# Optimization experiments

Hardware: AMD Instinct MI355X
Metric: run time of the kernel (lower is better)

The kernel has to match this reference:

```python
import math
import jax, jax.numpy as jnp
import numpy as np

NUM_HEADS = 16
D_MODEL = 1024
WINDOW = 512


def alibi_slopes(num_heads):
    # 1 / ((2**8)**((i+1)/num_heads))  for i in range(num_heads)
    x = (2.0 ** 8) ** (1.0 / num_heads)
    return jnp.asarray([1.0 / x ** (i + 1) for i in range(num_heads)], dtype=jnp.float32)


def setup_inputs() -> dict:
    key = jax.random.key(0)
    k1, k2 = jax.random.split(key)
    x = jax.random.normal(k1, (1, 4096, D_MODEL), dtype=jnp.float32)
    # scale weight like a trained init so softmax isn't saturated
    w_kqv = jax.random.normal(k2, (D_MODEL, 3 * D_MODEL), dtype=jnp.float32) * 0.02
    return {"x": x, "w_kqv": w_kqv}


def reference(x, w_kqv):
    B, S, D = x.shape
    H = NUM_HEADS
    hd = D // H
    scale = math.sqrt(D)  # module scales by sqrt(d_model), not sqrt(head_dim)

    kqv = x @ w_kqv                       # [B, S, 3D]
    k, q, v = jnp.split(kqv, 3, axis=-1)  # chunk order: key, query, value
    k = k.reshape(B, S, H, hd).transpose(0, 2, 1, 3)  # [B, H, S, hd]
    q = q.reshape(B, S, H, hd).transpose(0, 2, 1, 3)
    v = v.reshape(B, S, H, hd).transpose(0, 2, 1, 3)

    # ALiBi bias: m_h * (j - i)
    pos = jnp.arange(S)
    rel = pos[None, :] - pos[:, None]                  # [S, S] = x - y
    bias = alibi_slopes(H)[:, None, None] * rel.astype(jnp.float32)  # [H, S, S]

    score = jnp.einsum("bhqd,bhkd->bhqk", q, k) / scale + bias[None]

    # causal sliding-window mask: allow 0 <= i - j <= WINDOW
    dist = pos[:, None] - pos[None, :]                 # i - j
    mask = (dist >= 0) & (dist <= WINDOW)              # [S, S]
    score = jnp.where(mask[None, None], score, -jnp.inf)

    attn = jax.nn.softmax(score, axis=-1)
    out = jnp.einsum("bhqk,bhkd->bhqd", attn, v)       # [B, H, S, hd]
    out = out.transpose(0, 2, 1, 3).reshape(B, S, D)
    return out
```

## Files before the change

kernel.cpp:

```cpp
#include <hip/hip_runtime.h>
#include <hip/hip_bf16.h>

#define SEQ   4096
#define DM    1024
#define NH    16
#define HD    64
#define N3    3072
#define WIN   512

#define LOG2E 1.4426950408889634f

typedef __attribute__((ext_vector_type(8))) short short8;
typedef __attribute__((ext_vector_type(4))) short short4v;
typedef __attribute__((ext_vector_type(4))) float float4v;

__device__ __forceinline__ float bf16_bits_to_float(unsigned short u) {
  return __uint_as_float(((unsigned int)u) << 16);
}

typedef __attribute__((address_space(3))) void lds_void_t;
typedef __attribute__((address_space(1))) const void gbl_void_t;
__device__ __forceinline__ void async_copy16(void* lds_dst, const void* g_src) {
  __builtin_amdgcn_global_load_lds((gbl_void_t*)g_src, (lds_void_t*)lds_dst,
                                   16, 0, 0);
}

template <int NT>
__device__ __forceinline__ int detect_fp32(const unsigned short* __restrict__ probe,
                                           float* red) {
  const int t = threadIdx.x;
  float mx = 0.0f;
#pragma unroll
  for (int p = 0; p < 8; ++p) {
    float v = bf16_bits_to_float(probe[(t * 8 + p) * 2]);
    if (v != v) v = 1e38f;
    mx = fmaxf(mx, fabsf(v));
  }
  red[t] = mx;
  __syncthreads();
  for (int s = NT / 2; s > 0; s >>= 1) {
    if (t < s) red[t] = fmaxf(red[t], red[t + s]);
    __syncthreads();
  }
  const int fl = red[0] > 100.0f ? 1 : 0;
  __syncthreads();
  return fl;
}

__device__ __forceinline__ int detect_fp32_wave(
    const unsigned short* __restrict__ probe) {
  const int lane = threadIdx.x & 63;
  float mx = 0.0f;
#pragma unroll
  for (int p = 0; p < 8; ++p) {
    float v = bf16_bits_to_float(probe[(lane * 8 + p) * 2]);
    if (v != v) v = 1e38f;
    mx = fmaxf(mx, fabsf(v));
  }
  return __any(mx > 100.0f) ? 1 : 0;
}

__global__ __launch_bounds__(256) void prep(
    const void* __restrict__ x, const void* __restrict__ w,
    __hip_bfloat16* __restrict__ xb, __hip_bfloat16* __restrict__ wt) {
  __shared__ __hip_bfloat16 tile[64][66];
  __shared__ float red[256];
  const int t = threadIdx.x;
  if (blockIdx.x < 2048) {
    const int fl = detect_fp32<256>((const unsigned short*)x, red);
    const int i0 = (blockIdx.x * 256 + t) * 8;
    if (fl) {
      const float* xf = (const float*)x + i0;
      float4 f0 = *(const float4*)(xf);
      float4 f1 = *(const float4*)(xf + 4);
      __hip_bfloat16 tmp[8];
      tmp[0] = __float2bfloat16(f0.x); tmp[1] = __float2bfloat16(f0.y);
      tmp[2] = __float2bfloat16(f0.z); tmp[3] = __float2bfloat16(f0.w);
      tmp[4] = __float2bfloat16(f1.x); tmp[5] = __float2bfloat16(f1.y);
      tmp[6] = __float2bfloat16(f1.z); tmp[7] = __float2bfloat16(f1.w);
      *(uint4*)&xb[i0] = *(const uint4*)tmp;
    } else {
      *(uint4*)&xb[i0] = *(const uint4*)((const __hip_bfloat16*)x + i0);
    }
  } else {
    const int bid = blockIdx.x - 2048;
    const int fl = detect_fp32<256>((const unsigned short*)w, red);
    const int n0 = (bid % 48) * 64;
    const int k0 = (bid / 48) * 64;
    const int tx = t & 63, ty0 = t >> 6;
    if (fl) {
      const float* wf = (const float*)w;
#pragma unroll
      for (int p = 0; p < 16; ++p) {
        int row = ty0 + p * 4;
        tile[row][tx] = __float2bfloat16(wf[(k0 + row) * N3 + n0 + tx]);
      }
    } else {
      const __hip_bfloat16* wb = (const __hip_bfloat16*)w;
#pragma unroll
      for (int p = 0; p < 16; ++p) {
        int row = ty0 + p * 4;
        tile[row][tx] = wb[(k0 + row) * N3 + n0 + tx];
      }
    }
    __syncthreads();
#pragma unroll
    for (int r = 0; r < 2; ++r) {
      int oe = r * 2048 + t * 8;
      int nr = oe >> 6, kc = oe & 63;
      __hip_bfloat16 v[8];
#pragma unroll
      for (int e = 0; e < 8; ++e) v[e] = tile[kc + e][nr];
      *(uint4*)&wt[(n0 + nr) * DM + k0 + kc] = *(const uint4*)v;
    }
  }
}

__global__ __launch_bounds__(512, 2) void gemm_kqv(
    const __hip_bfloat16* __restrict__ A,
    const __hip_bfloat16* __restrict__ BT,
    __hip_bfloat16* __restrict__ C) {
  __shared__ __align__(16) __hip_bfloat16 As[2][2][128 * 32];
  __shared__ __align__(16) __hip_bfloat16 Bs[2][192 * 64];

  const int flat = blockIdx.y * 16 + blockIdx.x;
  const int swz  = (flat & 7) * 64 + (flat >> 3);
  const int m0 = (swz >> 4) * 128;
  const int n0 = (swz & 15) * 192;

  const int t = threadIdx.x;
  const int wave = t >> 6, lane = t & 63;
  const int wm = wave >> 2, wn = wave & 3;
  const int l15 = lane & 15, quad = lane >> 4;

  const int arow = t >> 2;
  const int acol = ((t & 3) ^ (arow & 3)) * 8;
  const long aoff = (long)(m0 + arow) * DM + acol;
  const int brow = t >> 3;
  const int bcol = ((t & 7) ^ (brow & 7)) * 8;
  const long boff0 = (long)(n0 +       brow) * DM + bcol;
  const long boff1 = (long)(n0 +  64 + brow) * DM + bcol;
  const long boff2 = (long)(n0 + 128 + brow) * DM + bcol;
  const int ldst = t * 16;

#define STAGE_B(buf, kt) do { \
    const int ko_ = (kt) * 64; \
    async_copy16((char*)Bs[buf]         + ldst, &BT[boff0 + ko_]); \
    async_copy16((char*)Bs[buf] +  8192 + ldst, &BT[boff1 + ko_]); \
    async_copy16((char*)Bs[buf] + 16384 + ldst, &BT[boff2 + ko_]); } while (0)
#define STAGE_A(buf, kt) do { \
    const int ko_ = (kt) * 64; \
    async_copy16((char*)As[buf][0] + ldst, &A[aoff + ko_]); \
    async_copy16((char*)As[buf][1] + ldst, &A[aoff + ko_ + 32]); } while (0)

  float4v acc[4][3] = {};

  STAGE_B(0, 0); STAGE_A(0, 0);
  asm volatile("s_waitcnt vmcnt(0)" ::: "memory");
  __builtin_amdgcn_s_barrier();

  for (int kt = 0; kt < 16; ++kt) {
    const int P = kt & 1, N = P ^ 1;
    short8 a[4], b[3];

#pragma unroll
    for (int h = 0; h < 2; ++h) {
      const char* Ap = (const char*)As[P][h];
      const char* Bp = (const char*)Bs[P];
#pragma unroll
      for (int mi = 0; mi < 4; ++mi) {
        const int row = wm * 64 + mi * 16 + l15;
        a[mi] = *(const short8*)(Ap + row * 64 + ((quad ^ (row & 3)) << 4));
      }
#pragma unroll
      for (int ni = 0; ni < 3; ++ni) {
        const int row = wn * 48 + ni * 16 + l15;
        b[ni] = *(const short8*)(Bp + row * 128 +
                                 ((((h << 2) + quad) ^ (row & 7)) << 4));
      }
      if (h == 0) {
        if (kt < 15) {
          STAGE_B(N, kt + 1);
          asm volatile("s_waitcnt vmcnt(3)" ::: "memory");
        } else {
          asm volatile("s_waitcnt vmcnt(0)" ::: "memory");
        }
      } else {
        if (kt < 15) STAGE_A(N, kt + 1);
        asm volatile("s_waitcnt vmcnt(1)" ::: "memory");
      }
      __builtin_amdgcn_s_barrier();
      __builtin_amdgcn_s_setprio(1);
#pragma unroll
      for (int mi = 0; mi < 4; ++mi)
#pragma unroll
        for (int ni = 0; ni < 3; ++ni)
          acc[mi][ni] = __builtin_amdgcn_mfma_f32_16x16x32_bf16(
              a[mi], b[ni], acc[mi][ni], 0, 0, 0);
      __builtin_amdgcn_s_setprio(0);
      __builtin_amdgcn_s_barrier();
    }
  }
#undef STAGE_A
#undef STAGE_B

#pragma unroll
  for (int mi = 0; mi < 4; ++mi)
#pragma unroll
    for (int ni = 0; ni < 3; ++ni)
#pragma unroll
      for (int r = 0; r < 4; ++r) {
        int row = m0 + wm * 64 + mi * 16 + quad * 4 + r;
        int col = n0 + wn * 48 + ni * 16 + l15;
        C[row * N3 + col] = __float2bfloat16(acc[mi][ni][r]);
      }
}

#define SWZ(row) (((((row) ^ ((row) >> 3))) & 7) << 4)

__global__ __launch_bounds__(256, 4) void attn(
    const __hip_bfloat16* __restrict__ kqv,
    const unsigned short* __restrict__ xprobe,
    void* __restrict__ out) {
  __shared__ __align__(16) __hip_bfloat16 Ks[2][64 * 64];
  __shared__ __align__(16) __hip_bfloat16 Vt[2][64 * 64];
  __shared__ __align__(16) __hip_bfloat16 Ps[64 * 64];

  const int fl = detect_fp32_wave(xprobe);
  const int h  = blockIdx.y;
  const int bx = blockIdx.x;
  const int i0 = 64 * ((bx & 7) * 8 + (bx >> 3));
  const int t    = threadIdx.x;
  const int wave = t >> 6, lane = t & 63;
  const int l15 = lane & 15, quad = lane >> 4;
  const float nslope2 = -exp2f(-0.5f * (float)(h + 1)) * LOG2E;
  const float qscale  = LOG2E / 32.0f;

  short8 aq[2];
#pragma unroll
  for (int ks2 = 0; ks2 < 2; ++ks2)
    aq[ks2] = *(const short8*)&kqv[(i0 + wave * 16 + l15) * N3 + DM + h * HD +
                                   ks2 * 32 + quad * 8];

  float4v o[4] = {};
  float lsum[4] = {0.f, 0.f, 0.f, 0.f};

  const int jlo  = max(0, i0 - WIN);
  const int nblk = (i0 + 64 - jlo) >> 6;

  const int krow0 = t >> 3, krow1 = (t >> 3) + 32, kd0 = (t & 7) * 8;
  const int kdst0 = krow0 * 128 + ((kd0 * 2) ^ SWZ(krow0));
  const int kdst1 = krow1 * 128 + ((kd0 * 2) ^ SWZ(krow1));
  const int rbase = t >> 3;
  const int vd0   = (t & 7) * 8;
  const int kA    = (rbase & 15) + ((rbase >> 4) << 5);
  const int vsig2 = ((rbase & 15) * 8) + ((rbase >> 4) * 4);

  uint4 kregA, kregB, vregA, vregB;
  kregA = *(const uint4*)&kqv[(jlo + krow0) * N3 + h * HD + kd0];
  kregB = *(const uint4*)&kqv[(jlo + krow1) * N3 + h * HD + kd0];
  vregA = *(const uint4*)&kqv[(jlo + kA) * N3 + 2 * DM + h * HD + vd0];
  vregB = *(const uint4*)&kqv[(jlo + kA + 16) * N3 + 2 * DM + h * HD + vd0];

  {
    *(uint4*)((char*)Ks[0] + kdst0) = kregA;
    *(uint4*)((char*)Ks[0] + kdst1) = kregB;
    const unsigned short* pa = (const unsigned short*)&vregA;
    const unsigned short* pb = (const unsigned short*)&vregB;
#pragma unroll
    for (int e = 0; e < 8; ++e) {
      unsigned int pack = (unsigned int)pa[e] | ((unsigned int)pb[e] << 16);
      *(unsigned int*)((char*)Vt[0] + (vd0 + e) * 128 + (vsig2 ^ SWZ(vd0 + e))) = pack;
    }
  }
  if (nblk > 1) {
    const int jn = jlo + 64;
    kregA = *(const uint4*)&kqv[(jn + krow0) * N3 + h * HD + kd0];
    kregB = *(const uint4*)&kqv[(jn + krow1) * N3 + h * HD + kd0];
    vregA = *(const uint4*)&kqv[(jn + kA) * N3 + 2 * DM + h * HD + vd0];
    vregB = *(const uint4*)&kqv[(jn + kA + 16) * N3 + 2 * DM + h * HD + vd0];
  }
  __syncthreads();

  for (int b = 0; b < nblk; ++b) {
    const int cur = b & 1, nxt = cur ^ 1;

    float4v sacc[4] = {};
#pragma unroll
    for (int ks2 = 0; ks2 < 2; ++ks2)
#pragma unroll
      for (int nt = 0; nt < 4; ++nt) {
        const int row = nt * 16 + l15;
        short8 bk = *(const short8*)((const char*)Ks[cur] + row * 128 +
                                     ((ks2 * 64 + quad * 16) ^ SWZ(row)));
        sacc[nt] = __builtin_amdgcn_mfma_f32_16x16x32_bf16(aq[ks2], bk, sacc[nt], 0, 0, 0);
      }

    const int dbase = (i0 + wave * 16 + quad * 4) - (jlo + b * 64 + l15);
    const float s16 = nslope2 * -16.0f;
#pragma unroll
    for (int r = 0; r < 4; ++r) {
      float bias = nslope2 * (float)(dbase + r);
      int rel = dbase + r;
      short4v pk;
      float ls = 0.0f;
#pragma unroll
      for (int nt = 0; nt < 4; ++nt) {
        float x = fmaf(sacc[nt][r], qscale, bias);
        x = ((unsigned)rel <= (unsigned)WIN) ? x : -200.0f;
        __hip_bfloat16 hb = __float2bfloat16(exp2f(x));
        unsigned short bits = *reinterpret_cast<const unsigned short*>(&hb);
        pk[nt] = (short)bits;
        ls += bf16_bits_to_float(bits);
        bias += s16;
        rel -= 16;
      }
      lsum[r] += ls;
      const int prow = wave * 16 + quad * 4 + r;
      *(short4v*)((char*)Ps + prow * 128 + ((l15 * 8) ^ SWZ(prow))) = pk;
    }

    if (b + 1 < nblk) {
      *(uint4*)((char*)Ks[nxt] + kdst0) = kregA;
      *(uint4*)((char*)Ks[nxt] + kdst1) = kregB;
      const unsigned short* pa = (const unsigned short*)&vregA;
      const unsigned short* pb = (const unsigned short*)&vregB;
#pragma unroll
      for (int e = 0; e < 8; ++e) {
        unsigned int pack = (unsigned int)pa[e] | ((unsigned int)pb[e] << 16);
        *(unsigned int*)((char*)Vt[nxt] + (vd0 + e) * 128 + (vsig2 ^ SWZ(vd0 + e))) = pack;
      }
      if (b + 2 < nblk) {
        const int jn = jlo + (b + 2) * 64;
        kregA = *(const uint4*)&kqv[(jn + krow0) * N3 + h * HD + kd0];
        kregB = *(const uint4*)&kqv[(jn + krow1) * N3 + h * HD + kd0];
        vregA = *(const uint4*)&kqv[(jn + kA) * N3 + 2 * DM + h * HD + vd0];
        vregB = *(const uint4*)&kqv[(jn + kA + 16) * N3 + 2 * DM + h * HD + vd0];
      }
    }

#pragma unroll
    for (int ks = 0; ks < 64; ks += 32) {
      const int prow = wave * 16 + l15;
      short8 ap = *(const short8*)((const char*)Ps + prow * 128 +
                                   ((ks * 2 + quad * 16) ^ SWZ(prow)));
#pragma unroll
      for (int dt = 0; dt < 4; ++dt) {
        const int vrow = dt * 16 + l15;
        short8 bv = *(const short8*)((const char*)Vt[cur] + vrow * 128 +
                                     ((ks * 2 + quad * 16) ^ SWZ(vrow)));
        o[dt] = __builtin_amdgcn_mfma_f32_16x16x32_bf16(ap, bv, o[dt], 0, 0, 0);
      }
    }

    __syncthreads();
  }

#pragma unroll
  for (int r = 0; r < 4; ++r) {
    float s = lsum[r];
    s += __shfl_xor(s, 1, 64);
    s += __shfl_xor(s, 2, 64);
    s += __shfl_xor(s, 4, 64);
    s += __shfl_xor(s, 8, 64);
    const float inv_l = 1.0f / s;
    const int row = i0 + wave * 16 + quad * 4 + r;
#pragma unroll
    for (int dt = 0; dt < 4; ++dt) {
      const int idx = row * DM + h * HD + dt * 16 + l15;
      const float v = o[dt][r] * inv_l;
      if (fl) ((float*)out)[idx] = v;
      else    ((__hip_bfloat16*)out)[idx] = __float2bfloat16(v);
    }
  }
}

extern "C" void kernel_launch(void* const* d_in, const int* in_sizes, int n_in,
                              void* d_out, int out_size, void* d_ws, size_t ws_size,
                              hipStream_t stream) {
  char* ws = (char*)d_ws;
  __hip_bfloat16* wt  = (__hip_bfloat16*)(ws + 4096);
  __hip_bfloat16* kqv = (__hip_bfloat16*)(ws + 4096 + 6291456);
  __hip_bfloat16* xb  = (__hip_bfloat16*)d_out;

  hipLaunchKernelGGL(prep, dim3(2048 + 768), dim3(256), 0, stream,
                     d_in[0], d_in[1], xb, wt);
  hipLaunchKernelGGL(gemm_kqv, dim3(16, 32), dim3(512), 0, stream, xb, wt, kqv);
  hipLaunchKernelGGL(attn, dim3(64, 16), dim3(256), 0, stream,
                     kqv, (const unsigned short*)d_in[0], d_out);
}
```

Baseline: 143.0 us.

## Fuse fp32-to-bf16 conversion of x into GEMM A-tile loading

Removes the separate pass that converted x to bf16 in the prep kernel. The GEMM now reads fp32 x directly into registers two k-tiles ahead, converts it to bf16 and writes it into LDS, with hand-placed waitcnt counts. This saves a full write and re-read of the bf16 copy of x. In exchange, the A operand can no longer use async LDS copies, register pressure rises, and each 128-row A tile is converted again by each of the 16 column blocks that reads it.

```diff
diff --git a/kernel.cpp b/kernel.cpp
--- a/kernel.cpp
+++ b/kernel.cpp
@@ -25,6 +25,18 @@
                                    16, 0, 0);
 }
 
+#define VMW(n) asm volatile("s_waitcnt vmcnt(" #n ")" ::: "memory")
+#define LGKM0() asm volatile("s_waitcnt lgkmcnt(0)" ::: "memory")
+
+__device__ __forceinline__ uint4 pack_bf16x8(float4 a, float4 b) {
+  __hip_bfloat16 h[8];
+  h[0] = __float2bfloat16(a.x); h[1] = __float2bfloat16(a.y);
+  h[2] = __float2bfloat16(a.z); h[3] = __float2bfloat16(a.w);
+  h[4] = __float2bfloat16(b.x); h[5] = __float2bfloat16(b.y);
+  h[6] = __float2bfloat16(b.z); h[7] = __float2bfloat16(b.w);
+  return *(const uint4*)h;
+}
+
 template <int NT>
 __device__ __forceinline__ int detect_fp32(const unsigned short* __restrict__ probe,
                                            float* red) {
@@ -61,68 +73,51 @@
 }
 
 __global__ __launch_bounds__(256) void prep(
-    const void* __restrict__ x, const void* __restrict__ w,
-    __hip_bfloat16* __restrict__ xb, __hip_bfloat16* __restrict__ wt) {
+    const void* __restrict__ w, __hip_bfloat16* __restrict__ wt) {
   __shared__ __hip_bfloat16 tile[64][66];
   __shared__ float red[256];
   const int t = threadIdx.x;
-  if (blockIdx.x < 2048) {
-    const int fl = detect_fp32<256>((const unsigned short*)x, red);
-    const int i0 = (blockIdx.x * 256 + t) * 8;
-    if (fl) {
-      const float* xf = (const float*)x + i0;
-      float4 f0 = *(const float4*)(xf);
-      float4 f1 = *(const float4*)(xf + 4);
-      __hip_bfloat16 tmp[8];
-      tmp[0] = __float2bfloat16(f0.x); tmp[1] = __float2bfloat16(f0.y);
-      tmp[2] = __float2bfloat16(f0.z); tmp[3] = __float2bfloat16(f0.w);
-      tmp[4] = __float2bfloat16(f1.x); tmp[5] = __float2bfloat16(f1.y);
-      tmp[6] = __float2bfloat16(f1.z); tmp[7] = __float2bfloat16(f1.w);
-      *(uint4*)&xb[i0] = *(const uint4*)tmp;
-    } else {
-      *(uint4*)&xb[i0] = *(const uint4*)((const __hip_bfloat16*)x + i0);
+  const int bid = blockIdx.x;
+  const int fl = detect_fp32<256>((const unsigned short*)w, red);
+  const int n0 = (bid % 48) * 64;
+  const int k0 = (bid / 48) * 64;
+  const int tx = t & 63, ty0 = t >> 6;
+  if (fl) {
+    const float* wf = (const float*)w;
+#pragma unroll
+    for (int p = 0; p < 16; ++p) {
+      int row = ty0 + p * 4;
+      tile[row][tx] = __float2bfloat16(wf[(k0 + row) * N3 + n0 + tx]);
     }
   } else {
-    const int bid = blockIdx.x - 2048;
-    const int fl = detect_fp32<256>((const unsigned short*)w, red);
-    const int n0 = (bid % 48) * 64;
-    const int k0 = (bid / 48) * 64;
-    const int tx = t & 63, ty0 = t >> 6;
-    if (fl) {
-      const float* wf = (const float*)w;
-#pragma unroll
-      for (int p = 0; p < 16; ++p) {
-        int row = ty0 + p * 4;
-        tile[row][tx] = __float2bfloat16(wf[(k0 + row) * N3 + n0 + tx]);
-      }
-    } else {
-      const __hip_bfloat16* wb = (const __hip_bfloat16*)w;
-#pragma unroll
-      for (int p = 0; p < 16; ++p) {
-        int row = ty0 + p * 4;
-        tile[row][tx] = wb[(k0 + row) * N3 + n0 + tx];
-      }
-    }
-    __syncthreads();
-#pragma unroll
-    for (int r = 0; r < 2; ++r) {
-      int oe = r * 2048 + t * 8;
-      int nr = oe >> 6, kc = oe & 63;
-      __hip_bfloat16 v[8];
-#pragma unroll
-      for (int e = 0; e < 8; ++e) v[e] = tile[kc + e][nr];
-      *(uint4*)&wt[(n0 + nr) * DM + k0 + kc] = *(const uint4*)v;
-    }
+    const __hip_bfloat16* wb = (const __hip_bfloat16*)w;
+#pragma unroll
+    for (int p = 0; p < 16; ++p) {
+      int row = ty0 + p * 4;
+      tile[row][tx] = wb[(k0 + row) * N3 + n0 + tx];
+    }
+  }
+  __syncthreads();
+#pragma unroll
+  for (int r = 0; r < 2; ++r) {
+    int oe = r * 2048 + t * 8;
+    int nr = oe >> 6, kc = oe & 63;
+    __hip_bfloat16 v[8];
+#pragma unroll
+    for (int e = 0; e < 8; ++e) v[e] = tile[kc + e][nr];
+    *(uint4*)&wt[(n0 + nr) * DM + k0 + kc] = *(const uint4*)v;
   }
 }
 
 __global__ __launch_bounds__(512, 2) void gemm_kqv(
-    const __hip_bfloat16* __restrict__ A,
+    const void* __restrict__ xin,
     const __hip_bfloat16* __restrict__ BT,
     __hip_bfloat16* __restrict__ C) {
   __shared__ __align__(16) __hip_bfloat16 As[2][2][128 * 32];
   __shared__ __align__(16) __hip_bfloat16 Bs[2][192 * 64];
 
+  const int fl = detect_fp32_wave((const unsigned short*)xin);
+
   const int flat = blockIdx.y * 16 + blockIdx.x;
   const int swz  = (flat & 7) * 64 + (flat >> 3);
   const int m0 = (swz >> 4) * 128;
@@ -135,7 +130,6 @@
 
   const int arow = t >> 2;
   const int acol = ((t & 3) ^ (arow & 3)) * 8;
-  const long aoff = (long)(m0 + arow) * DM + acol;
   const int brow = t >> 3;
   const int bcol = ((t & 7) ^ (brow & 7)) * 8;
   const long boff0 = (long)(n0 +       brow) * DM + bcol;
@@ -150,45 +144,61 @@
     async_copy16((char*)Bs[buf] + 16384 + ldst, &BT[boff2 + ko_]); } while (0)
 #define STAGE_A(buf, kt) do { \
     const int ko_ = (kt) * 64; \
-    async_copy16((char*)As[buf][0] + ldst, &A[aoff + ko_]); \
-    async_copy16((char*)As[buf][1] + ldst, &A[aoff + ko_ + 32]); } while (0)
+    async_copy16((char*)As[buf][0] + ldst, &Ab[aoff + ko_]); \
+    async_copy16((char*)As[buf][1] + ldst, &Ab[aoff + ko_ + 32]); } while (0)
 
   float4v acc[4][3] = {};
 
-  STAGE_B(0, 0); STAGE_A(0, 0);
-  asm volatile("s_waitcnt vmcnt(0)" ::: "memory");
-  __builtin_amdgcn_s_barrier();
-
-  for (int kt = 0; kt < 16; ++kt) {
-    const int P = kt & 1, N = P ^ 1;
-    short8 a[4], b[3];
-
-#pragma unroll
-    for (int h = 0; h < 2; ++h) {
-      const char* Ap = (const char*)As[P][h];
-      const char* Bp = (const char*)Bs[P];
+  if (fl) {
+    const float* ax = (const float*)xin + (long)(m0 + arow) * DM + acol;
+    float4 la[2][4];
+
+    {
+      float4 r0 = *(const float4*)(ax + 0);
+      float4 r1 = *(const float4*)(ax + 4);
+      float4 r2 = *(const float4*)(ax + 32);
+      float4 r3 = *(const float4*)(ax + 36);
+      STAGE_B(0, 0);
+      la[1][0] = *(const float4*)(ax + 64);
+      la[1][1] = *(const float4*)(ax + 68);
+      la[1][2] = *(const float4*)(ax + 96);
+      la[1][3] = *(const float4*)(ax + 100);
+      VMW(7);
+      *(uint4*)((char*)As[0][0] + ldst) = pack_bf16x8(r0, r1);
+      *(uint4*)((char*)As[0][1] + ldst) = pack_bf16x8(r2, r3);
+      VMW(4);
+      LGKM0();
+      __builtin_amdgcn_s_barrier();
+    }
+
+#pragma unroll
+    for (int kt = 0; kt < 16; ++kt) {
+      const int P = kt & 1, N = P ^ 1;
+      short8 a[4], b[3];
+
 #pragma unroll
       for (int mi = 0; mi < 4; ++mi) {
         const int row = wm * 64 + mi * 16 + l15;
-        a[mi] = *(const short8*)(Ap + row * 64 + ((quad ^ (row & 3)) << 4));
+        a[mi] = *(const short8*)((const char*)As[P][0] + row * 64 +
+                                 ((quad ^ (row & 3)) << 4));
       }
 #pragma unroll
       for (int ni = 0; ni < 3; ++ni) {
         const int row = wn * 48 + ni * 16 + l15;
-        b[ni] = *(const short8*)(Bp + row * 128 +
-                                 ((((h << 2) + quad) ^ (row & 7)) << 4));
-      }
-      if (h == 0) {
-        if (kt < 15) {
-          STAGE_B(N, kt + 1);
-          asm volatile("s_waitcnt vmcnt(3)" ::: "memory");
-        } else {
-          asm volatile("s_waitcnt vmcnt(0)" ::: "memory");
-        }
-      } else {
-        if (kt < 15) STAGE_A(N, kt + 1);
-        asm volatile("s_waitcnt vmcnt(1)" ::: "memory");
-      }
+        b[ni] = *(const short8*)((const char*)Bs[P] + row * 128 +
+                                 ((quad ^ (row & 7)) << 4));
+      }
+      if (kt < 15) STAGE_B(N, kt + 1);
+      if (kt < 14) {
+        const float* a2 = ax + (kt + 2) * 64;
+        la[P][0] = *(const float4*)(a2 + 0);
+        la[P][1] = *(const float4*)(a2 + 4);
+        la[P][2] = *(const float4*)(a2 + 32);
+        la[P][3] = *(const float4*)(a2 + 36);
+      }
+      if (kt < 14)      VMW(7);
+      else if (kt == 14) VMW(3);
+      else               VMW(0);
       __builtin_amdgcn_s_barrier();
       __builtin_amdgcn_s_setprio(1);
 #pragma unroll
@@ -199,6 +209,86 @@
               a[mi], b[ni], acc[mi][ni], 0, 0, 0);
       __builtin_amdgcn_s_setprio(0);
       __builtin_amdgcn_s_barrier();
+
+#pragma unroll
+      for (int mi = 0; mi < 4; ++mi) {
+        const int row = wm * 64 + mi * 16 + l15;
+        a[mi] = *(const short8*)((const char*)As[P][1] + row * 64 +
+                                 ((quad ^ (row & 3)) << 4));
+      }
+#pragma unroll
+      for (int ni = 0; ni < 3; ++ni) {
+        const int row = wn * 48 + ni * 16 + l15;
+        b[ni] = *(const short8*)((const char*)Bs[P] + row * 128 +
+                                 (((4 + quad) ^ (row & 7)) << 4));
+      }
+      if (kt < 15) {
+        *(uint4*)((char*)As[N][0] + ldst) = pack_bf16x8(la[N][0], la[N][1]);
+        *(uint4*)((char*)As[N][1] + ldst) = pack_bf16x8(la[N][2], la[N][3]);
+      }
+      if (kt < 14) VMW(4);
+      else         VMW(0);
+      LGKM0();
+      __builtin_amdgcn_s_barrier();
+      __builtin_amdgcn_s_setprio(1);
+#pragma unroll
+      for (int mi = 0; mi < 4; ++mi)
+#pragma unroll
+        for (int ni = 0; ni < 3; ++ni)
+          acc[mi][ni] = __builtin_amdgcn_mfma_f32_16x16x32_bf16(
+              a[mi], b[ni], acc[mi][ni], 0, 0, 0);
+      __builtin_amdgcn_s_setprio(0);
+      __builtin_amdgcn_s_barrier();
+    }
+  } else {
+    const __hip_bfloat16* Ab = (const __hip_bfloat16*)xin;
+    const long aoff = (long)(m0 + arow) * DM + acol;
+
+    STAGE_B(0, 0); STAGE_A(0, 0);
+    asm volatile("s_waitcnt vmcnt(0)" ::: "memory");
+    __builtin_amdgcn_s_barrier();
+
+    for (int kt = 0; kt < 16; ++kt) {
+      const int P = kt & 1, N = P ^ 1;
+      short8 a[4], b[3];
+
+#pragma unroll
+      for (int h = 0; h < 2; ++h) {
+        const char* Ap = (const char*)As[P][h];
+        const char* Bp = (const char*)Bs[P];
+#pragma unroll
+        for (int mi = 0; mi < 4; ++mi) {
+          const int row = wm * 64 + mi * 16 + l15;
+          a[mi] = *(const short8*)(Ap + row * 64 + ((quad ^ (row & 3)) << 4));
+        }
+#pragma unroll
+        for (int ni = 0; ni < 3; ++ni) {
+          const int row = wn * 48 + ni * 16 + l15;
+          b[ni] = *(const short8*)(Bp + row * 128 +
+                                   ((((h << 2) + quad) ^ (row & 7)) << 4));
+        }
+        if (h == 0) {
+          if (kt < 15) {
+            STAGE_B(N, kt + 1);
+            VMW(3);
+          } else {
+            VMW(0);
+          }
+        } else {
+          if (kt < 15) STAGE_A(N, kt + 1);
+          VMW(1);
+        }
+        __builtin_amdgcn_s_barrier();
+        __builtin_amdgcn_s_setprio(1);
+#pragma unroll
+        for (int mi = 0; mi < 4; ++mi)
+#pragma unroll
+          for (int ni = 0; ni < 3; ++ni)
+            acc[mi][ni] = __builtin_amdgcn_mfma_f32_16x16x32_bf16(
+                a[mi], b[ni], acc[mi][ni], 0, 0, 0);
+        __builtin_amdgcn_s_setprio(0);
+        __builtin_amdgcn_s_barrier();
+      }
     }
   }
 #undef STAGE_A
@@ -381,11 +471,10 @@
   char* ws = (char*)d_ws;
   __hip_bfloat16* wt  = (__hip_bfloat16*)(ws + 4096);
   __hip_bfloat16* kqv = (__hip_bfloat16*)(ws + 4096 + 6291456);
-  __hip_bfloat16* xb  = (__hip_bfloat16*)d_out;
-
-  hipLaunchKernelGGL(prep, dim3(2048 + 768), dim3(256), 0, stream,
-                     d_in[0], d_in[1], xb, wt);
-  hipLaunchKernelGGL(gemm_kqv, dim3(16, 32), dim3(512), 0, stream, xb, wt, kqv);
+
+  hipLaunchKernelGGL(prep, dim3(768), dim3(256), 0, stream, d_in[1], wt);
+  hipLaunchKernelGGL(gemm_kqv, dim3(16, 32), dim3(512), 0, stream,
+                     d_in[0], wt, kqv);
   hipLaunchKernelGGL(attn, dim3(64, 16), dim3(256), 0, stream,
                      kqv, (const unsigned short*)d_in[0], d_out);
 }
```

After: 163.3 us. 1.14x slower.
